# Kernel optimization log

Hardware: AMD Instinct MI355X
Metric: run time of the kernel (lower is better)

## Reference

```python
import jax, jax.numpy as jnp
import numpy as np

# Static hyperparams matching init_kwargs
KSIZE, STRIDE, PAD, DIL = 3, 2, 1, 1


def setup_inputs() -> dict:
    key = jax.random.key(0)
    k1, k2 = jax.random.split(key)
    B, H, W, Cin, Cout = 8, 128, 128, 128, 256
    feats = jax.random.normal(k1, (B * H * W, Cin), dtype=jnp.float32)
    weight = jax.random.normal(k2, (KSIZE * KSIZE, Cin, Cout), dtype=jnp.float32) * 0.05
    alpha_upper = jnp.ones((1,), dtype=jnp.float32)
    # dense grid coords [N, 3] = (batch, y, x), matching a dense image sparse tensor
    bb, yy, xx = np.meshgrid(np.arange(B), np.arange(H), np.arange(W), indexing='ij')
    coords = jnp.asarray(np.stack([bb, yy, xx], -1).reshape(-1, 3), dtype=jnp.int32)
    return {"feats": feats, "weight": weight, "alpha_upper": alpha_upper,
            "coords": coords, "H": H, "W": W, "B": B}


def _coord_ranges(H, W):
    # Faithful translation of WrappedMinkowskiStridedOperation.__init__ + forward
    # coordinate math, specialized to a dense grid (per-batch min=0, max=H-1/W-1).
    kernel_origin = DIL * ((KSIZE - 1) // 2) * (KSIZE % 2)
    dilated = DIL * (KSIZE - 1) + 1
    ks_off = kernel_origin - dilated + 1          # _kernel_start_offset
    ke_off = kernel_origin                        # _kernel_end_offset
    idx_start = kernel_origin - PAD               # _index_start_offset
    ranges = []
    for ext in (H, W):
        idx_end = (ext - 1) + kernel_origin + PAD - dilated + 2
        start = max(idx_start, (0 + ks_off - idx_start) // STRIDE * STRIDE + idx_start)
        end = min(idx_end, ((ext - 1 + ke_off - idx_start) // STRIDE + 1) * STRIDE + idx_start)
        ranges.append(np.arange(start, end, STRIDE))
    offsets = np.arange(KSIZE) * DIL - kernel_origin  # kernel region offsets
    return ranges[0], ranges[1], offsets, idx_start


def reference(feats, weight, alpha_upper, coords, H, W, B):
    Cin = feats.shape[1]
    Cout = weight.shape[-1]
    ys, xs, offs, idx_start = _coord_ranges(H, W)
    OH, OW = len(ys), len(xs)
    oy, ox = jnp.meshgrid(jnp.asarray(ys, jnp.int32), jnp.asarray(xs, jnp.int32), indexing='ij')
    dy, dx = np.meshgrid(offs, offs, indexing='ij')
    dy = jnp.asarray(dy.reshape(-1), jnp.int32)  # [kvol]
    dx = jnp.asarray(dx.reshape(-1), jnp.int32)
    ny = oy[None] + dy[:, None, None]            # [kvol, OH, OW]
    nx = ox[None] + dx[:, None, None]
    valid = (ny >= 0) & (ny < H) & (nx >= 0) & (nx < W)
    lin = jnp.clip(ny, 0, H - 1) * W + jnp.clip(nx, 0, W - 1)  # [kvol, OH, OW]
    feats3 = feats.reshape(B, H * W, Cin)
    gathered = feats3[:, lin]                    # [B, kvol, OH, OW, Cin]
    gathered = jnp.where(valid[None, ..., None], gathered, jnp.zeros((), feats.dtype))
    out = jnp.einsum('bkhwc,kcd->bhwd', gathered, weight)  # [B, OH, OW, Cout]
    out_feats = out.reshape(B * OH * OW, Cout)
    # output coordinates, remapped as in forward (shift by index_start, divide by stride)
    oc = jnp.stack([oy, ox], -1).reshape(-1, 2)  # [OH*OW, 2]
    oc = (oc - jnp.int32(idx_start)) // jnp.int32(STRIDE)
    oc = jnp.tile(oc, (B, 1))
    bcol = jnp.repeat(jnp.arange(B, dtype=jnp.int32), OH * OW)
    out_coords = jnp.concatenate([bcol[:, None], oc], axis=1)
    return out_feats, out_coords, alpha_upper
```

## Files before the change

### kernel.cpp

```cpp
#include <hip/hip_runtime.h>


#define OUT_FEATS_ELEMS (32768 * 256)
#define OUT_COORDS_OFF  OUT_FEATS_ELEMS
#define ALPHA_OFF       (OUT_FEATS_ELEMS + 32768 * 3)

#define BW_BYTES   (18 * 16384)

typedef float v16f __attribute__((ext_vector_type(16)));

__device__ __forceinline__ unsigned pk4fp8(float a, float b, float c, float d) {
    unsigned u = 0;
    u = __builtin_amdgcn_cvt_pk_fp8_f32(a, b, u, false);
    u = __builtin_amdgcn_cvt_pk_fp8_f32(c, d, u, true);
    return u;
}

#define GLOAD_LDS16(SRC, DST)                                                  \
    __builtin_amdgcn_global_load_lds(                                          \
        (const __attribute__((address_space(1))) void*)(SRC),                  \
        (__attribute__((address_space(3))) void*)(DST), 16, 0, 0)

#define WAITBAR_(N) asm volatile("s_waitcnt vmcnt(" #N ")\n\ts_barrier" ::: "memory")
#define WAITBAR(N)  WAITBAR_(N)
#define BAR()       asm volatile("s_barrier" ::: "memory")

__global__ void wprep_kernel(const float* __restrict__ w,
                             const float* __restrict__ alpha,
                             unsigned char* __restrict__ Bw,
                             float* __restrict__ out) {
    int cid = blockIdx.x * 256 + threadIdx.x;
    if (cid < 32768) {
        int b = cid >> 12, iy = (cid >> 6) & 63, ix = cid & 63;
        float* c = out + OUT_COORDS_OFF + (size_t)cid * 3;
        c[0] = (float)b; c[1] = (float)iy; c[2] = (float)ix;
        if (cid == 0) out[ALPHA_OFF] = alpha[0];
    }
    if (cid < 18432) {
        int ch  = cid & 7;
        int row = (cid >> 3) & 127;
        int t   = cid >> 10;
        int nb  = (t >= 9) ? 1 : 0;
        int tap = t - 9 * nb;
        int chp = ch ^ (row & 7);
        int hb  = (row >> 3) & 1;
        int n   = (nb << 7) + row;
        int kb  = (tap << 7) + (chp << 4);
        unsigned u[4];
#pragma unroll
        for (int q = 0; q < 4; ++q) {
            int kq = kb + 4 * (q ^ (hb << 1));
            float f0 = w[(size_t)(kq + 0) * 256 + n];
            float f1 = w[(size_t)(kq + 1) * 256 + n];
            float f2 = w[(size_t)(kq + 2) * 256 + n];
            float f3 = w[(size_t)(kq + 3) * 256 + n];
            u[q] = pk4fp8(f0, f1, f2, f3);
        }
        uint4 r; r.x = u[0]; r.y = u[1]; r.z = u[2]; r.w = u[3];
        *(uint4*)(Bw + (size_t)cid * 16) = r;
    }
}

__global__ void coords_alpha_kernel(float* __restrict__ out, const float* __restrict__ alpha) {
    int i = blockIdx.x * 256 + threadIdx.x;
    int b = i >> 12, iy = (i >> 6) & 63, ix = i & 63;
    float* c = out + OUT_COORDS_OFF + (size_t)i * 3;
    c[0] = (float)b; c[1] = (float)iy; c[2] = (float)ix;
    if (i == 0) out[ALPHA_OFF] = alpha[0];
}

__global__ __launch_bounds__(512, 4) void gemm_conv_kernel(
    const float* __restrict__ feats,
    const unsigned char* __restrict__ Bw,
    float* __restrict__ out)
{
    __shared__ unsigned char Aband[3 * 128 * 128];
    __shared__ unsigned char Bs[256 * 128];

    const int tid  = threadIdx.x;
    const int bid  = blockIdx.x;
    const int my   = ((bid & 7) << 6) + ((bid >> 3) & 63);
    const int m0   = my << 6;
    const int bb   = my >> 6;
    const int iy   = my & 63;

    const int lane = tid & 63, wave = tid >> 6;
    const int wm   = (wave >> 2) << 5;
    const int wn   = (wave & 3) << 6;
    const int l31  = lane & 31;
    const int hh   = lane >> 5;
    const int xorl = l31 & 7;
    const int bhalf = (hh ^ ((l31 >> 3) & 1)) << 3;

    const unsigned char* bsrc0 = Bw + ((size_t)((wave >> 2) * 9) << 14)
                                    + ((size_t)(wave & 3) << 12) + ((size_t)lane << 4);
    auto stageB = [&](int tap) {
        const unsigned char* bs = bsrc0 + ((size_t)tap << 14);
        unsigned char* bdst = Bs + (wave << 12);
#pragma unroll
        for (int q = 0; q < 4; ++q)
            GLOAD_LDS16(bs + (q << 10), bdst + (q << 10));
    };

    stageB(0);

    const int ny0 = (iy << 1) - 1;
    auto issueRow = [&](int r, float4* f) {
        const int ny = ny0 + r;
#pragma unroll
        for (int it = 0; it < 8; ++it) {
            const int idx = (it << 9) + tid;
            const int nx  = idx >> 5;
            const int c4  = (idx & 31) << 2;
            f[it] = *(const float4*)(feats +
                ((((size_t)(bb << 14) + ny * 128 + nx)) << 7) + c4);
        }
    };
    auto writeRow = [&](int r, const float4* f) {
#pragma unroll
        for (int it = 0; it < 8; ++it) {
            const int idx = (it << 9) + tid;
            const int nx  = idx >> 5;
            const int c4  = (idx & 31) << 2;
            const unsigned u = pk4fp8(f[it].x, f[it].y, f[it].z, f[it].w);
            const int key4 = ((nx + 1) >> 1) & 15;
            const int boff = ((r * 128 + nx) << 7)
                + (((c4 >> 4) ^ (key4 & 7)) << 4)
                + (((((c4 >> 3) & 1) ^ (key4 >> 3)) & 1) << 3)
                + (c4 & 7);
            *(unsigned*)(Aband + boff) = u;
        }
    };

    if (iy == 0) {
        for (int z = tid; z < 1024; z += 512) {
            uint4 zz; zz.x = 0u; zz.y = 0u; zz.z = 0u; zz.w = 0u;
            *(uint4*)(Aband + z * 16) = zz;
        }
    }
    {
        float4 fA[8], fB[8];
        const int r0 = (iy == 0) ? 1 : 0;
        issueRow(r0, fA);
        issueRow(r0 + 1, fB);
        writeRow(r0, fA);
        issueRow(2, fA);
        writeRow(r0 + 1, fB);
        writeRow(2, fA);
    }
    __syncthreads();

    v16f acc[2];
#pragma unroll
    for (int j = 0; j < 2; j++) acc[j] = (v16f)(0.0f);

    auto computeTap = [&](int dy, int dx) {
        const int r   = dy + 1;
        const int ixv = wm + l31;
        const int nxq = (ixv << 1) + dx;
        const bool pad = (nxq < 0);
        const int nxs = pad ? 0 : nxq;
        const int key4 = ((nxq + 1) >> 1) & 15;
        const int abase = ((r * 128 + nxs) << 7) + ((hh ^ (key4 >> 3)) << 3);
        const int kc = key4 & 7;
#pragma unroll
        for (int seg = 0; seg < 8; ++seg) {
            long long a0 = *(const long long*)(Aband + abase + ((seg ^ kc) << 4));
            if (pad) a0 = 0LL;
            long long b2[2];
#pragma unroll
            for (int j = 0; j < 2; j++)
                b2[j] = *(const long long*)(Bs + ((wn + (j << 5) + l31) << 7)
                                            + ((seg ^ xorl) << 4) + bhalf);
            __builtin_amdgcn_s_setprio(1);
#pragma unroll
            for (int j = 0; j < 2; j++)
                acc[j] = __builtin_amdgcn_mfma_f32_32x32x16_fp8_fp8(a0, b2[j], acc[j], 0, 0, 0);
            __builtin_amdgcn_s_setprio(0);
        }
    };

#pragma unroll
    for (int tap = 0; tap < 9; ++tap) {
        computeTap(tap / 3 - 1, tap % 3 - 1);
        if (tap < 8) {
            BAR();
            stageB(tap + 1);
            WAITBAR(0);
        }
    }

#pragma unroll
    for (int j = 0; j < 2; j++) {
        const int gcol = wn + (j << 5) + l31;
#pragma unroll
        for (int r = 0; r < 16; ++r) {
            const int grow = m0 + wm + (r & 3) + ((r >> 2) << 3) + (hh << 2);
            __builtin_nontemporal_store(acc[j][r], &out[(size_t)grow * 256 + gcol]);
        }
    }
}

__global__ void naive_conv_kernel(const float* __restrict__ feats,
                                  const float* __restrict__ w,
                                  float* __restrict__ out) {
    int m = blockIdx.x;
    int n = threadIdx.x;
    int bb = m >> 12, iy = (m >> 6) & 63, ix = m & 63;
    float acc = 0.f;
    for (int tap = 0; tap < 9; ++tap) {
        int ny = 2 * iy + tap / 3 - 1;
        int nx = 2 * ix + tap % 3 - 1;
        if ((unsigned)ny < 128u && (unsigned)nx < 128u) {
            const float* fr = feats + ((size_t)((bb << 14) + (ny << 7) + nx) << 7);
            const float* wr = w + tap * 32768 + n;
            for (int c = 0; c < 128; ++c) acc += fr[c] * wr[c * 256];
        }
    }
    out[(size_t)m * 256 + n] = acc;
}

extern "C" void kernel_launch(void* const* d_in, const int* in_sizes, int n_in,
                              void* d_out, int out_size, void* d_ws, size_t ws_size,
                              hipStream_t stream) {
    const float* feats  = (const float*)d_in[0];
    const float* weight = (const float*)d_in[1];
    const float* alpha  = (const float*)d_in[2];
    float* out = (float*)d_out;

    const size_t NEED = (size_t)BW_BYTES;
    if (ws_size >= NEED) {
        unsigned char* Bw = (unsigned char*)d_ws;
        wprep_kernel<<<144, 256, 0, stream>>>(weight, alpha, Bw, out);
        gemm_conv_kernel<<<512, 512, 0, stream>>>(feats, Bw, out);
    } else {
        coords_alpha_kernel<<<128, 256, 0, stream>>>(out, alpha);
        naive_conv_kernel<<<32768, 256, 0, stream>>>(feats, weight, out);
    }
}
```

Baseline: 128.2 us.

## Load weight fragments straight into registers with double buffering, dropping LDS B staging

Weights are repacked into a per-lane MFMA fragment layout, so each lane loads its B operands for a tap directly from global memory (L2) into registers. A two-buffer register pipeline prefetches the next tap while the current one computes. This removes the B shared-memory tile and the per-tap barriers and global-to-LDS copies. In exchange it adds 32 long-long registers per thread and repeated global reads of the weights by every block, relying on caches to serve them.

```diff
diff --git a/kernel.cpp b/kernel.cpp
--- a/kernel.cpp
+++ b/kernel.cpp
@@ -5,7 +5,7 @@
 #define OUT_COORDS_OFF  OUT_FEATS_ELEMS
 #define ALPHA_OFF       (OUT_FEATS_ELEMS + 32768 * 3)
 
-#define BW_BYTES   (18 * 16384)
+#define BW2_BYTES  (9 * 8 * 4096)
 
 typedef float v16f __attribute__((ext_vector_type(16)));
 
@@ -16,18 +16,9 @@
     return u;
 }
 
-#define GLOAD_LDS16(SRC, DST)                                                  \
-    __builtin_amdgcn_global_load_lds(                                          \
-        (const __attribute__((address_space(1))) void*)(SRC),                  \
-        (__attribute__((address_space(3))) void*)(DST), 16, 0, 0)
-
-#define WAITBAR_(N) asm volatile("s_waitcnt vmcnt(" #N ")\n\ts_barrier" ::: "memory")
-#define WAITBAR(N)  WAITBAR_(N)
-#define BAR()       asm volatile("s_barrier" ::: "memory")
-
 __global__ void wprep_kernel(const float* __restrict__ w,
                              const float* __restrict__ alpha,
-                             unsigned char* __restrict__ Bw,
+                             unsigned char* __restrict__ Bw2,
                              float* __restrict__ out) {
     int cid = blockIdx.x * 256 + threadIdx.x;
     if (cid < 32768) {
@@ -36,28 +27,22 @@
         c[0] = (float)b; c[1] = (float)iy; c[2] = (float)ix;
         if (cid == 0) out[ALPHA_OFF] = alpha[0];
     }
-    if (cid < 18432) {
-        int ch  = cid & 7;
-        int row = (cid >> 3) & 127;
-        int t   = cid >> 10;
-        int nb  = (t >= 9) ? 1 : 0;
-        int tap = t - 9 * nb;
-        int chp = ch ^ (row & 7);
-        int hb  = (row >> 3) & 1;
-        int n   = (nb << 7) + row;
-        int kb  = (tap << 7) + (chp << 4);
-        unsigned u[4];
-#pragma unroll
-        for (int q = 0; q < 4; ++q) {
-            int kq = kb + 4 * (q ^ (hb << 1));
-            float f0 = w[(size_t)(kq + 0) * 256 + n];
-            float f1 = w[(size_t)(kq + 1) * 256 + n];
-            float f2 = w[(size_t)(kq + 2) * 256 + n];
-            float f3 = w[(size_t)(kq + 3) * 256 + n];
-            u[q] = pk4fp8(f0, f1, f2, f3);
-        }
-        uint4 r; r.x = u[0]; r.y = u[1]; r.z = u[2]; r.w = u[3];
-        *(uint4*)(Bw + (size_t)cid * 16) = r;
+    {
+        const int l31 = cid & 31;
+        const int hh  = (cid >> 5) & 1;
+        const int n32 = (cid >> 6) & 7;
+        const int seg = (cid >> 9) & 7;
+        const int tap = cid >> 12;
+        const int n   = (n32 << 5) + l31;
+        const int kb  = (tap << 7) + (seg << 4) + (hh << 3);
+        float f[8];
+#pragma unroll
+        for (int q = 0; q < 8; ++q)
+            f[q] = w[(size_t)(kb + q) * 256 + n];
+        uint2 r;
+        r.x = pk4fp8(f[0], f[1], f[2], f[3]);
+        r.y = pk4fp8(f[4], f[5], f[6], f[7]);
+        *(uint2*)(Bw2 + (size_t)cid * 8) = r;
     }
 }
 
@@ -71,11 +56,10 @@
 
 __global__ __launch_bounds__(512, 4) void gemm_conv_kernel(
     const float* __restrict__ feats,
-    const unsigned char* __restrict__ Bw,
+    const unsigned char* __restrict__ Bw2,
     float* __restrict__ out)
 {
     __shared__ unsigned char Aband[3 * 128 * 128];
-    __shared__ unsigned char Bs[256 * 128];
 
     const int tid  = threadIdx.x;
     const int bid  = blockIdx.x;
@@ -89,20 +73,14 @@
     const int wn   = (wave & 3) << 6;
     const int l31  = lane & 31;
     const int hh   = lane >> 5;
-    const int xorl = l31 & 7;
-    const int bhalf = (hh ^ ((l31 >> 3) & 1)) << 3;
-
-    const unsigned char* bsrc0 = Bw + ((size_t)((wave >> 2) * 9) << 14)
-                                    + ((size_t)(wave & 3) << 12) + ((size_t)lane << 4);
-    auto stageB = [&](int tap) {
-        const unsigned char* bs = bsrc0 + ((size_t)tap << 14);
-        unsigned char* bdst = Bs + (wave << 12);
-#pragma unroll
-        for (int q = 0; q < 4; ++q)
-            GLOAD_LDS16(bs + (q << 10), bdst + (q << 10));
-    };
-
-    stageB(0);
+
+    const unsigned char* bbase = Bw2 + ((size_t)(wn >> 5) << 9) + ((size_t)lane << 3);
+
+    long long bA[16], bB[16];
+#define LOADB(T, BUF)                                                          \
+    _Pragma("unroll")                                                          \
+    for (int s = 0; s < 16; ++s)                                               \
+        BUF[s] = *(const long long*)(bbase + (T) * 32768 + (s & 7) * 4096 + (s >> 3) * 512);
 
     const int ny0 = (iy << 1) - 1;
     auto issueRow = [&](int r, float4* f) {
@@ -148,13 +126,14 @@
         writeRow(r0 + 1, fB);
         writeRow(2, fA);
     }
+    LOADB(0, bA);
     __syncthreads();
 
     v16f acc[2];
 #pragma unroll
     for (int j = 0; j < 2; j++) acc[j] = (v16f)(0.0f);
 
-    auto computeTap = [&](int dy, int dx) {
+    auto computeTap = [&](const long long* buf, int dy, int dx) {
         const int r   = dy + 1;
         const int ixv = wm + l31;
         const int nxq = (ixv << 1) + dx;
@@ -167,28 +146,24 @@
         for (int seg = 0; seg < 8; ++seg) {
             long long a0 = *(const long long*)(Aband + abase + ((seg ^ kc) << 4));
             if (pad) a0 = 0LL;
-            long long b2[2];
+            __builtin_amdgcn_s_setprio(1);
 #pragma unroll
             for (int j = 0; j < 2; j++)
-                b2[j] = *(const long long*)(Bs + ((wn + (j << 5) + l31) << 7)
-                                            + ((seg ^ xorl) << 4) + bhalf);
-            __builtin_amdgcn_s_setprio(1);
-#pragma unroll
-            for (int j = 0; j < 2; j++)
-                acc[j] = __builtin_amdgcn_mfma_f32_32x32x16_fp8_fp8(a0, b2[j], acc[j], 0, 0, 0);
+                acc[j] = __builtin_amdgcn_mfma_f32_32x32x16_fp8_fp8(
+                    a0, buf[(j << 3) + seg], acc[j], 0, 0, 0);
             __builtin_amdgcn_s_setprio(0);
         }
     };
 
-#pragma unroll
-    for (int tap = 0; tap < 9; ++tap) {
-        computeTap(tap / 3 - 1, tap % 3 - 1);
-        if (tap < 8) {
-            BAR();
-            stageB(tap + 1);
-            WAITBAR(0);
-        }
-    }
+    LOADB(1, bB); computeTap(bA, -1, -1);
+    LOADB(2, bA); computeTap(bB, -1,  0);
+    LOADB(3, bB); computeTap(bA, -1,  1);
+    LOADB(4, bA); computeTap(bB,  0, -1);
+    LOADB(5, bB); computeTap(bA,  0,  0);
+    LOADB(6, bA); computeTap(bB,  0,  1);
+    LOADB(7, bB); computeTap(bA,  1, -1);
+    LOADB(8, bA); computeTap(bB,  1,  0);
+    computeTap(bA,  1,  1);
 
 #pragma unroll
     for (int j = 0; j < 2; j++) {
@@ -199,6 +174,7 @@
             __builtin_nontemporal_store(acc[j][r], &out[(size_t)grow * 256 + gcol]);
         }
     }
+#undef LOADB
 }
 
 __global__ void naive_conv_kernel(const float* __restrict__ feats,
@@ -228,11 +204,11 @@
     const float* alpha  = (const float*)d_in[2];
     float* out = (float*)d_out;
 
-    const size_t NEED = (size_t)BW_BYTES;
+    const size_t NEED = (size_t)BW2_BYTES;
     if (ws_size >= NEED) {
-        unsigned char* Bw = (unsigned char*)d_ws;
-        wprep_kernel<<<144, 256, 0, stream>>>(weight, alpha, Bw, out);
-        gemm_conv_kernel<<<512, 512, 0, stream>>>(feats, Bw, out);
+        unsigned char* Bw2 = (unsigned char*)d_ws;
+        wprep_kernel<<<144, 256, 0, stream>>>(weight, alpha, Bw2, out);
+        gemm_conv_kernel<<<512, 512, 0, stream>>>(feats, Bw2, out);
     } else {
         coords_alpha_kernel<<<128, 256, 0, stream>>>(out, alpha);
         naive_conv_kernel<<<32768, 256, 0, stream>>>(feats, weight, out);
```

After: 151.1 us. +17.8%, slower.
